# Kernel optimization log

Measured on AMD Instinct MI355X. Metric: run time of the kernel, lower is better.

The kernel has to match this reference:

```python
import jax, jax.numpy as jnp
import numpy as np

K_WIN = 7  # temporal window size (odd)
EPS = 1e-5


def setup_inputs() -> dict:
    key = jax.random.key(0)
    ks = jax.random.split(key, 10)
    B, C, T, H, W = 8, 512, 32, 7, 7
    N, E = 8, 64  # heads, inter channels = C // N
    s = 0.02
    return {
        "x": jax.random.normal(ks[0], (B, C, T, H, W), jnp.float32),
        "gamma": jnp.ones((C,), jnp.float32),
        "beta": jnp.zeros((C,), jnp.float32),
        "Wq": jax.random.normal(ks[1], (N, E, C), jnp.float32) * s,
        "bq": jax.random.normal(ks[2], (N, E), jnp.float32) * s,
        "Wk": jax.random.normal(ks[3], (N, E, C), jnp.float32) * s,
        "bk": jax.random.normal(ks[4], (N, E), jnp.float32) * s,
        "Wv": jax.random.normal(ks[5], (N, E, C), jnp.float32) * s,
        "bv": jax.random.normal(ks[6], (N, E), jnp.float32) * s,
        "Wo": jax.random.normal(ks[7], (N, C, E), jnp.float32) * s,
        "bo": jax.random.normal(ks[8], (N, C), jnp.float32) * s,
    }


def reference(x, gamma, beta, Wq, bq, Wk, bk, Wv, bv, Wo, bo):
    B, C, T, H, W = x.shape
    K = K_WIN
    P = H * W          # spatial positions per frame
    L = K * P          # positions per temporal window

    # BatchNorm3d (training-mode batch stats over B,T,H,W)
    mean = jnp.mean(x, axis=(0, 2, 3, 4), keepdims=True)
    var = jnp.var(x, axis=(0, 2, 3, 4), keepdims=True)
    g = gamma[None, :, None, None, None]
    b = beta[None, :, None, None, None]
    xb = g * (x - mean) * jax.lax.rsqrt(var + EPS) + b  # (B,C,T,H,W)

    # temporal zero-pad so that number of windows S == T
    pad = K // 2
    xp = jnp.pad(xb, ((0, 0), (0, 0), (pad, pad), (0, 0), (0, 0)))
    # gather sliding windows: (B,C,T,K,H,W)
    win_idx = jnp.arange(T)[:, None] + jnp.arange(K)[None, :]
    xw = xp[:, :, win_idx]

    xwf = xw.reshape(B, C, T, L)   # window tokens (key/value source)
    xcf = xb.reshape(B, C, T, P)   # center frame (query source)

    # per-head projections (dropout is identity in eval mode)
    q = jnp.einsum('nec,bctp->bntep', Wq, xcf) + bq[None, :, None, :, None]
    k = jnp.einsum('nec,bctl->bntel', Wk, xwf) + bk[None, :, None, :, None]
    v = jnp.einsum('nec,bctl->bntel', Wv, xwf) + bv[None, :, None, :, None]

    # attention: scores (B,N,T,P,L), softmax over window positions L (no scaling, as in original)
    alpha = jnp.einsum('bntep,bntel->bntpl', q, k)
    alpha = jax.nn.softmax(alpha, axis=-1)
    y = jnp.einsum('bntpl,bntel->bntep', alpha, v)

    # output projection per head, then mean over heads
    out = jnp.einsum('nce,bntep->bntcp', Wo, y) + bo[None, :, None, :, None]
    z = jnp.mean(out, axis=1)                 # (B,T,C,P)
    z = jnp.transpose(z, (0, 2, 1, 3)).reshape(B, C, T, H, W)
    return z + xb  # residual with BN output
```

## Files before the change

kernel.cpp:

```cpp
#include <hip/hip_runtime.h>
#include <hip/hip_bf16.h>


typedef float f32x4 __attribute__((ext_vector_type(4)));
typedef short s16x8 __attribute__((ext_vector_type(8)));
typedef short s16x4 __attribute__((ext_vector_type(4)));
typedef __bf16 bf16x8 __attribute__((ext_vector_type(8)));

static __device__ __forceinline__ float bf2f(unsigned short u){
  union { unsigned int i; float f; } x; x.i = ((unsigned int)u) << 16; return x.f;
}
static __device__ __forceinline__ unsigned short f2bf(float f){
  union { __hip_bfloat16 h; unsigned short u; } x; x.h = __float2bfloat16(f); return x.u;
}
static __device__ __forceinline__ f32x4 mfma16(s16x8 a, s16x8 b, f32x4 c){
  return __builtin_amdgcn_mfma_f32_16x16x32_bf16(
      __builtin_bit_cast(bf16x8, a), __builtin_bit_cast(bf16x8, b), c, 0, 0, 0);
}
static __device__ __forceinline__ void gload16(const unsigned short* g, unsigned short* l){
  __builtin_amdgcn_global_load_lds(
      (const __attribute__((address_space(1))) unsigned int*)g,
      (__attribute__((address_space(3))) unsigned int*)l, 16, 0, 0);
}
#define VMCNT(N) asm volatile("s_waitcnt vmcnt(" #N ")" ::: "memory")

__global__ __launch_bounds__(256) void stats_kernel(const float* __restrict__ x,
    const float* __restrict__ gamma, const float* __restrict__ beta,
    float* __restrict__ scale, float* __restrict__ shift){
  const int c = blockIdx.x, tid = threadIdx.x;
  float s1 = 0.f, s2 = 0.f;
  const float* xc = x + (size_t)c*1568;
  for (int i = tid; i < 3136; i += 256){
    int b = i / 392, j = i - b*392;
    f32x4 v = *(const f32x4*)(xc + (size_t)b*802816 + j*4);
    s1 += v[0]+v[1]+v[2]+v[3];
    s2 += v[0]*v[0]+v[1]*v[1]+v[2]*v[2]+v[3]*v[3];
  }
  #pragma unroll
  for (int off = 32; off > 0; off >>= 1){
    s1 += __shfl_down(s1, off);
    s2 += __shfl_down(s2, off);
  }
  __shared__ float r1[4], r2[4];
  int wave = tid >> 6, lane = tid & 63;
  if (lane == 0){ r1[wave] = s1; r2[wave] = s2; }
  __syncthreads();
  if (tid == 0){
    float t1 = r1[0]+r1[1]+r1[2]+r1[3];
    float t2 = r2[0]+r2[1]+r2[2]+r2[3];
    const float inv = 1.f/12544.f;
    float mean = t1*inv;
    float var  = t2*inv - mean*mean;
    float sc = gamma[c]*rsqrtf(var + 1e-5f);
    scale[c] = sc;
    shift[c] = beta[c] - mean*sc;
  }
}

__global__ __launch_bounds__(512) void pack_kernel(const float* __restrict__ Wq,
    const float* __restrict__ Wk, const float* __restrict__ Wv,
    const float* __restrict__ Wo, const float* __restrict__ bo,
    unsigned short* __restrict__ Wall, unsigned short* __restrict__ Wo2,
    float* __restrict__ bo_sum){
  int i = blockIdx.x*512 + threadIdx.x;
  if (i < 786432){
    const float* W = (i < 262144) ? Wq : (i < 524288 ? Wk : Wv);
    Wall[i] = f2bf(W[i & 262143]);
  } else if (i < 1048576){
    int j = i - 786432;
    int c = j >> 9, k = j & 511, nn = k >> 6, e = k & 63;
    Wo2[j] = f2bf(Wo[((size_t)nn*512 + c)*64 + e] * 0.125f);
  } else if (i < 1049088){
    int c = i - 1048576;
    float s = 0.f;
    #pragma unroll
    for (int nn = 0; nn < 8; ++nn) s += bo[nn*512 + c];
    bo_sum[c] = s * 0.125f;
  }
}

__global__ __launch_bounds__(256) void xt_kernel(const float* __restrict__ x,
    const float* __restrict__ scale, const float* __restrict__ shift,
    unsigned short* __restrict__ Xt){
  __shared__ unsigned short Xc[512][52];
  const int bt = blockIdx.x, b = bt >> 5, t = bt & 31, tid = threadIdx.x;
  const float* xb = x + (size_t)b*802816 + t*49;
  for (int i = tid; i < 512*49; i += 256){
    int c = i / 49, p = i - c*49;
    Xc[c][p] = f2bf(xb[(size_t)c*1568 + p]*scale[c] + shift[c]);
  }
  __syncthreads();
  unsigned short* dst = Xt + (size_t)bt*32768;
  for (int i = tid; i < 4096; i += 256){
    int p = i & 63, c0 = (i >> 6) << 3;
    s16x8 v;
    #pragma unroll
    for (int j = 0; j < 8; ++j) v[j] = (p < 49) ? (short)Xc[c0+j][p] : (short)0;
    *(s16x8*)(dst + p*512 + c0) = v;
  }
}

__global__ __launch_bounds__(256) void qkv_gemm(const unsigned short* __restrict__ Wall,
    const unsigned short* __restrict__ Xt,
    const float* __restrict__ bq, const float* __restrict__ bk, const float* __restrict__ bv,
    unsigned short* __restrict__ Qg, unsigned short* __restrict__ Kg,
    unsigned short* __restrict__ Vg){
  __shared__ unsigned short As[4][4096];
  __shared__ unsigned short Bs[4][4096];
  const int bid = blockIdx.x;
  const int id = (bid & 7)*192 + (bid >> 3);
  const int bm = id % 12, bn = id / 12;
  const int m0 = bm*128, n0 = bn*128;
  const int tid = threadIdx.x;
  const int w = __builtin_amdgcn_readfirstlane(tid >> 6);
  const int lane = tid & 63, l15 = lane & 15, g = lane >> 4, g4 = (lane >> 4)*4;
  const int wm = w >> 1, wn = w & 1;
  const int cA = w*128 + lane;
  int offA[4], offB[4];
  #pragma unroll
  for (int mi = 0; mi < 4; ++mi){
    int row = wm*64 + mi*16 + l15;
    offA[mi] = row*32 + ((g ^ ((row>>1)&3))<<3);
  }
  #pragma unroll
  for (int ni = 0; ni < 4; ++ni){
    int col = wn*64 + ni*16 + l15;
    offB[ni] = col*32 + ((g ^ ((col>>1)&3))<<3);
  }
  f32x4 acc[4][4];
  #pragma unroll
  for (int mi = 0; mi < 4; ++mi)
    #pragma unroll
    for (int ni = 0; ni < 4; ++ni) acc[mi][ni] = 0.f;

  auto stage = [&](int bufi, int ks){
    #pragma unroll
    for (int it = 0; it < 2; ++it){
      int c = cA + it*64;
      int row = c >> 2, slot = c & 3;
      int ko = ks*32 + ((slot ^ ((row>>1)&3))<<3);
      gload16(Wall + (size_t)(m0 + row)*512 + ko, &As[bufi][(w*128 + it*64)*8]);
      gload16(Xt   + (size_t)(n0 + row)*512 + ko, &Bs[bufi][(w*128 + it*64)*8]);
    }
  };
  auto compute = [&](int bufi){
    s16x8 Af[4], Bf[4];
    #pragma unroll
    for (int mi = 0; mi < 4; ++mi) Af[mi] = *(const s16x8*)&As[bufi][offA[mi]];
    #pragma unroll
    for (int ni = 0; ni < 4; ++ni) Bf[ni] = *(const s16x8*)&Bs[bufi][offB[ni]];
    #pragma unroll
    for (int mi = 0; mi < 4; ++mi)
      #pragma unroll
      for (int ni = 0; ni < 4; ++ni)
        acc[mi][ni] = mfma16(Af[mi], Bf[ni], acc[mi][ni]);
  };

  stage(0, 0); stage(1, 1); stage(2, 2);
  #pragma unroll 1
  for (int j = 0; j < 13; ++j){
    VMCNT(8);
    __builtin_amdgcn_s_barrier();
    __builtin_amdgcn_sched_barrier(0);
    stage((j+3) & 3, j+3);
    __builtin_amdgcn_s_setprio(1);
    compute(j & 3);
    __builtin_amdgcn_s_setprio(0);
  }
  VMCNT(8);  __builtin_amdgcn_s_barrier(); __builtin_amdgcn_sched_barrier(0);
  __builtin_amdgcn_s_setprio(1); compute(1); __builtin_amdgcn_s_setprio(0);
  VMCNT(4);  __builtin_amdgcn_s_barrier(); __builtin_amdgcn_sched_barrier(0);
  __builtin_amdgcn_s_setprio(1); compute(2); __builtin_amdgcn_s_setprio(0);
  VMCNT(0);  __builtin_amdgcn_s_barrier(); __builtin_amdgcn_sched_barrier(0);
  __builtin_amdgcn_s_setprio(1); compute(3); __builtin_amdgcn_s_setprio(0);

  const int qb = bm*2 + wm;
  const int which = qb >> 3, n = qb & 7;
  const int bt = bn*2 + wn, b = bt >> 5, t = bt & 31;
  const size_t bnt = ((size_t)(b*8 + n)*32 + t);
  const float* bias = which == 0 ? bq : (which == 1 ? bk : bv);
  #pragma unroll
  for (int mi = 0; mi < 4; ++mi){
    const int e0 = mi*16 + g4;
    const f32x4 bb = *(const f32x4*)(bias + n*64 + e0);
    #pragma unroll
    for (int ni = 0; ni < 4; ++ni){
      const int p = ni*16 + l15;
      f32x4 v = acc[mi][ni] + bb;
      if (which == 0) v *= 1.4426950408889634f;
      if (p < 49){
        if (which < 2){
          s16x4 u;
          #pragma unroll
          for (int r = 0; r < 4; ++r) u[r] = (short)f2bf(v[r]);
          *(s16x4*)((which == 0 ? Qg : Kg) + (bnt*49 + p)*64 + e0) = u;
        } else {
          #pragma unroll
          for (int r = 0; r < 4; ++r)
            Vg[bnt*3328 + (size_t)(e0 + r)*52 + p] = f2bf(v[r]);
        }
      }
    }
  }
}

__global__ __launch_bounds__(512,2) void attn_kernel(const unsigned short* __restrict__ Qg,
    const unsigned short* __restrict__ Kg, const unsigned short* __restrict__ Vg,
    const float* __restrict__ bk, const float* __restrict__ bv,
    unsigned short* __restrict__ Yg){
  const int bid = blockIdx.x;
  const int bt = ((bid & 7) << 5) | (bid >> 3);
  const int b = bt >> 5, t = bt & 31, tid = threadIdx.x;
  const int n = __builtin_amdgcn_readfirstlane(tid >> 6);
  const int lane = tid & 63, g = lane >> 4, l15 = lane & 15, g4 = (lane >> 4)*4;
  const size_t bnt = ((size_t)(b*8 + n)*32 + t);
  const unsigned short* Qb = Qg + bnt*3136;
  s16x8 Qf[4][2];
  #pragma unroll
  for (int ni = 0; ni < 4; ++ni)
    #pragma unroll
    for (int ks = 0; ks < 2; ++ks)
      Qf[ni][ks] = *(const s16x8*)(Qb + (ni*16 + l15)*64 + ks*32 + g*8);
  const float* bkp = bk + n*64;
  f32x4 bkf[2][2];
  bkf[0][0] = *(const f32x4*)(bkp + g*8);      bkf[0][1] = *(const f32x4*)(bkp + g*8 + 4);
  bkf[1][0] = *(const f32x4*)(bkp + 32 + g*8); bkf[1][1] = *(const f32x4*)(bkp + 32 + g*8 + 4);
  float pad_l[4];
  #pragma unroll
  for (int ni = 0; ni < 4; ++ni){
    float s = 0.f;
    #pragma unroll
    for (int ks = 0; ks < 2; ++ks)
      #pragma unroll
      for (int h = 0; h < 2; ++h)
        #pragma unroll
        for (int j = 0; j < 4; ++j)
          s += bf2f((unsigned short)Qf[ni][ks][h*4+j]) * bkf[ks][h][j];
    s += __shfl_xor(s, 16); s += __shfl_xor(s, 32);
    pad_l[ni] = s;
  }
  float m_run[4], d_run[4];
  f32x4 Yacc[4][4];
  #pragma unroll
  for (int ni = 0; ni < 4; ++ni){
    m_run[ni] = -1e30f; d_run[ni] = 0.f;
    #pragma unroll
    for (int me = 0; me < 4; ++me) Yacc[me][ni] = 0.f;
  }
  int slo = 3 - t; if (slo < 0) slo = 0;
  int shi = 34 - t; if (shi > 6) shi = 6;
  for (int s = slo; s <= shi; ++s){
    const int tt = t + s - 3;
    const unsigned short* Kb = Kg + ((size_t)(b*8 + n)*32 + tt)*3136;
    const unsigned short* Vb = Vg + ((size_t)(b*8 + n)*32 + tt)*3328;
    f32x4 S[4][4];
    #pragma unroll
    for (int mi = 0; mi < 4; ++mi)
      #pragma unroll
      for (int ni = 0; ni < 4; ++ni) S[mi][ni] = 0.f;
    __builtin_amdgcn_s_setprio(1);
    #pragma unroll
    for (int ks = 0; ks < 2; ++ks)
      #pragma unroll
      for (int mi = 0; mi < 4; ++mi){
        s16x8 Kf = *(const s16x8*)(Kb + (mi*16 + l15)*64 + ks*32 + g*8);
        #pragma unroll
        for (int ni = 0; ni < 4; ++ni)
          S[mi][ni] = mfma16(Kf, Qf[ni][ks], S[mi][ni]);
      }
    __builtin_amdgcn_s_setprio(0);
    #pragma unroll
    for (int r = 0; r < 4; ++r){
      const bool bad = (g4 + r) >= 1;
      #pragma unroll
      for (int ni = 0; ni < 4; ++ni)
        S[3][ni][r] = bad ? -1e30f : S[3][ni][r];
    }
    #pragma unroll
    for (int ni = 0; ni < 4; ++ni){
      float mx = -1e30f;
      #pragma unroll
      for (int mi = 0; mi < 4; ++mi)
        #pragma unroll
        for (int r = 0; r < 4; ++r) mx = fmaxf(mx, S[mi][ni][r]);
      mx = fmaxf(mx, __shfl_xor(mx, 16));
      mx = fmaxf(mx, __shfl_xor(mx, 32));
      const float mn = fmaxf(m_run[ni], mx);
      const float rs = exp2f(m_run[ni] - mn);
      m_run[ni] = mn;
      float sum = 0.f;
      #pragma unroll
      for (int mi = 0; mi < 4; ++mi)
        #pragma unroll
        for (int r = 0; r < 4; ++r){
          float e = exp2f(S[mi][ni][r] - mn);
          S[mi][ni][r] = e; sum += e;
        }
      sum += __shfl_xor(sum, 16); sum += __shfl_xor(sum, 32);
      d_run[ni] = d_run[ni]*rs + sum;
      #pragma unroll
      for (int me = 0; me < 4; ++me) Yacc[me][ni] *= rs;
    }
    #pragma unroll
    for (int ks = 0; ks < 2; ++ks){
      s16x8 Pf[4];
      #pragma unroll
      for (int ni = 0; ni < 4; ++ni){
        f32x4 a = S[2*ks][ni], b2 = S[2*ks+1][ni];
        s16x8 pf;
        #pragma unroll
        for (int j = 0; j < 4; ++j){
          pf[j]   = (short)f2bf(a[j]);
          pf[4+j] = (short)f2bf(b2[j]);
        }
        Pf[ni] = pf;
      }
      __builtin_amdgcn_s_setprio(1);
      #pragma unroll
      for (int me = 0; me < 4; ++me){
        s16x4 vlo = *(const s16x4*)(Vb + (size_t)(me*16 + l15)*52 + ks*32 + g4);
        s16x4 vhi = *(const s16x4*)(Vb + (size_t)(me*16 + l15)*52 + ks*32 + 16 + g4);
        s16x8 Vf;
        #pragma unroll
        for (int j = 0; j < 4; ++j){ Vf[j] = vlo[j]; Vf[4+j] = vhi[j]; }
        #pragma unroll
        for (int ni = 0; ni < 4; ++ni)
          Yacc[me][ni] = mfma16(Vf, Pf[ni], Yacc[me][ni]);
      }
      __builtin_amdgcn_s_setprio(0);
    }
  }
  const int n_pad = slo + (6 - shi);
  f32x4 bvf[4];
  #pragma unroll
  for (int me = 0; me < 4; ++me)
    bvf[me] = *(const f32x4*)(bv + n*64 + me*16 + g4);
  unsigned short* Yb = Yg + bnt*3136;
  #pragma unroll
  for (int ni = 0; ni < 4; ++ni){
    float rs = 1.f, pw = 0.f, d = d_run[ni];
    if (n_pad > 0){
      const float mf = fmaxf(m_run[ni], pad_l[ni]);
      rs = exp2f(m_run[ni] - mf);
      pw = (float)(n_pad*49) * exp2f(pad_l[ni] - mf);
      d = d_run[ni]*rs + pw;
    }
    const float inv = 1.f/d;
    const int p = ni*16 + l15;
    if (p < 49){
      #pragma unroll
      for (int me = 0; me < 4; ++me){
        s16x4 u;
        #pragma unroll
        for (int r = 0; r < 4; ++r)
          u[r] = (short)f2bf((Yacc[me][ni][r]*rs + pw*bvf[me][r])*inv);
        *(s16x4*)(Yb + (size_t)p*64 + me*16 + g4) = u;
      }
    }
  }
}

__global__ __launch_bounds__(256) void out_gemm(const unsigned short* __restrict__ Wo2,
    const unsigned short* __restrict__ Yg, const unsigned short* __restrict__ Xt,
    const float* __restrict__ scale, const float* __restrict__ shift,
    const float* __restrict__ bo_sum, float* __restrict__ out){
  __shared__ unsigned short As[4][4096];
  __shared__ unsigned short Bs[4][4096];
  const int bid = blockIdx.x;
  const int id = (bid & 7)*64 + (bid >> 3);
  const int bm = id % 4, bn = id / 4;
  const int m0 = bm*128, n0 = bn*128;
  const int tid = threadIdx.x;
  const int w = __builtin_amdgcn_readfirstlane(tid >> 6);
  const int lane = tid & 63, l15 = lane & 15, g = lane >> 4, g4 = (lane >> 4)*4;
  const int wm = w >> 1, wn = w & 1;
  const int cA = w*128 + lane;
  int offA[4], offB[4];
  #pragma unroll
  for (int mi = 0; mi < 4; ++mi){
    int row = wm*64 + mi*16 + l15;
    offA[mi] = row*32 + ((g ^ ((row>>1)&3))<<3);
  }
  #pragma unroll
  for (int ni = 0; ni < 4; ++ni){
    int col = wn*64 + ni*16 + l15;
    offB[ni] = col*32 + ((g ^ ((col>>1)&3))<<3);
  }
  f32x4 acc[4][4];
  #pragma unroll
  for (int mi = 0; mi < 4; ++mi)
    #pragma unroll
    for (int ni = 0; ni < 4; ++ni) acc[mi][ni] = 0.f;

  auto stage = [&](int bufi, int ks){
    const int nh = ks >> 1, eo = (ks & 1)*32;
    #pragma unroll
    for (int it = 0; it < 2; ++it){
      int c = cA + it*64;
      int row = c >> 2, slot = c & 3;
      int sw = ((slot ^ ((row>>1)&3))<<3);
      gload16(Wo2 + (size_t)(m0 + row)*512 + ks*32 + sw, &As[bufi][(w*128 + it*64)*8]);
      const int col = n0 + row, btc = col >> 6, p = col & 63;
      const size_t bb = ((size_t)((btc >> 5)*8 + nh)*32 + (btc & 31));
      gload16(Yg + bb*3136 + p*64 + eo + sw, &Bs[bufi][(w*128 + it*64)*8]);
    }
  };
  auto compute = [&](int bufi){
    s16x8 Af[4], Bf[4];
    #pragma unroll
    for (int mi = 0; mi < 4; ++mi) Af[mi] = *(const s16x8*)&As[bufi][offA[mi]];
    #pragma unroll
    for (int ni = 0; ni < 4; ++ni) Bf[ni] = *(const s16x8*)&Bs[bufi][offB[ni]];
    #pragma unroll
    for (int mi = 0; mi < 4; ++mi)
      #pragma unroll
      for (int ni = 0; ni < 4; ++ni)
        acc[mi][ni] = mfma16(Af[mi], Bf[ni], acc[mi][ni]);
  };

  stage(0, 0); stage(1, 1); stage(2, 2);
  #pragma unroll 1
  for (int j = 0; j < 13; ++j){
    VMCNT(8);
    __builtin_amdgcn_s_barrier();
    __builtin_amdgcn_sched_barrier(0);
    stage((j+3) & 3, j+3);
    __builtin_amdgcn_s_setprio(1);
    compute(j & 3);
    __builtin_amdgcn_s_setprio(0);
  }
  VMCNT(8);  __builtin_amdgcn_s_barrier(); __builtin_amdgcn_sched_barrier(0);
  __builtin_amdgcn_s_setprio(1); compute(1); __builtin_amdgcn_s_setprio(0);
  VMCNT(4);  __builtin_amdgcn_s_barrier(); __builtin_amdgcn_sched_barrier(0);
  __builtin_amdgcn_s_setprio(1); compute(2); __builtin_amdgcn_s_setprio(0);
  VMCNT(0);  __builtin_amdgcn_s_barrier(); __builtin_amdgcn_sched_barrier(0);
  __builtin_amdgcn_s_setprio(1); compute(3); __builtin_amdgcn_s_setprio(0);

  const int cb = m0 + wm*64;
  const int bt = bn*2 + wn, b = bt >> 5, t = bt & 31;
  const unsigned short* XtB = Xt + (size_t)bt*32768;
  #pragma unroll
  for (int mi = 0; mi < 4; ++mi){
    const int c0 = cb + mi*16 + g4;
    const f32x4 sc = *(const f32x4*)(bo_sum + c0);
    #pragma unroll
    for (int ni = 0; ni < 4; ++ni){
      const int p = ni*16 + l15;
      if (p < 49){
        s16x4 xb = *(const s16x4*)(XtB + p*512 + c0);
        #pragma unroll
        for (int r = 0; r < 4; ++r){
          const int c = c0 + r;
          out[((size_t)(b*512 + c))*1568 + t*49 + p] =
              acc[mi][ni][r] + sc[r] + bf2f((unsigned short)xb[r]);
        }
      }
    }
  }
}

extern "C" void kernel_launch(void* const* d_in, const int* in_sizes, int n_in_,
                              void* d_out, int out_size, void* d_ws, size_t ws_size,
                              hipStream_t stream){
  const float* x     = (const float*)d_in[0];
  const float* gamma = (const float*)d_in[1];
  const float* beta  = (const float*)d_in[2];
  const float* Wq    = (const float*)d_in[3];
  const float* bq    = (const float*)d_in[4];
  const float* Wk    = (const float*)d_in[5];
  const float* bk    = (const float*)d_in[6];
  const float* Wv    = (const float*)d_in[7];
  const float* bv    = (const float*)d_in[8];
  const float* Wo    = (const float*)d_in[9];
  const float* bo    = (const float*)d_in[10];
  float* out = (float*)d_out;

  char* ws = (char*)d_ws;
  float* scale  = (float*)ws;
  float* shift  = scale + 512;
  float* bo_sum = shift + 512;
  unsigned short* Wall = (unsigned short*)(ws + 8192);
  const size_t PAD = 16384;
  unsigned short* Wo2 = Wall + 786432;
  unsigned short* Xt  = Wo2 + 262144;
  unsigned short* Qg  = Xt + 8388608;
  unsigned short* Kg  = Qg + 6422528 + PAD;
  unsigned short* Vg  = Kg + 6422528 + PAD;
  unsigned short* Yg  = Vg + 6815744 + PAD;

  hipLaunchKernelGGL(stats_kernel, dim3(512), dim3(256), 0, stream,
                     x, gamma, beta, scale, shift);
  hipLaunchKernelGGL(pack_kernel, dim3(2049), dim3(512), 0, stream,
                     Wq, Wk, Wv, Wo, bo, Wall, Wo2, bo_sum);
  hipLaunchKernelGGL(xt_kernel, dim3(256), dim3(256), 0, stream,
                     x, scale, shift, Xt);
  hipLaunchKernelGGL(qkv_gemm, dim3(1536), dim3(256), 0, stream,
                     Wall, Xt, bq, bk, bv, Qg, Kg, Vg);
  hipLaunchKernelGGL(attn_kernel, dim3(256), dim3(512), 0, stream,
                     Qg, Kg, Vg, bk, bv, Yg);
  hipLaunchKernelGGL(out_gemm, dim3(512), dim3(256), 0, stream,
                     Wo2, Yg, Xt, scale, shift, bo_sum, out);
}
```

Measured before the change: 130.7 us.

## Enlarge QKV GEMM tile to 256x128 and switch both GEMMs to 3-stage pipelines

The QKV GEMM now computes a 256x128 output tile per block, with each wave holding 8x4 MFMA accumulators, so each staged X tile is reused across twice as many weight rows and the grid halves. Both GEMMs move from a 4-buffer to a 3-buffer LDS ring with a two-stage prefetch and request two blocks per CU via launch bounds. Together these cut LDS footprint and global B-operand traffic. In exchange they add register pressure from the larger accumulator, give less latency hiding per block, and leave fewer blocks to balance across CUs.

```diff
diff --git a/kernel.cpp b/kernel.cpp
--- a/kernel.cpp
+++ b/kernel.cpp
@@ -100,26 +100,25 @@
   }
 }
 
-__global__ __launch_bounds__(256) void qkv_gemm(const unsigned short* __restrict__ Wall,
+__global__ __launch_bounds__(256,2) void qkv_gemm(const unsigned short* __restrict__ Wall,
     const unsigned short* __restrict__ Xt,
     const float* __restrict__ bq, const float* __restrict__ bk, const float* __restrict__ bv,
     unsigned short* __restrict__ Qg, unsigned short* __restrict__ Kg,
     unsigned short* __restrict__ Vg){
-  __shared__ unsigned short As[4][4096];
-  __shared__ unsigned short Bs[4][4096];
+  __shared__ unsigned short As[3][8192];
+  __shared__ unsigned short Bs[3][4096];
   const int bid = blockIdx.x;
-  const int id = (bid & 7)*192 + (bid >> 3);
-  const int bm = id % 12, bn = id / 12;
-  const int m0 = bm*128, n0 = bn*128;
+  const int id = (bid & 7)*96 + (bid >> 3);
+  const int bm = id % 6, bn = id / 6;
+  const int m0 = bm*256, n0 = bn*128;
   const int tid = threadIdx.x;
   const int w = __builtin_amdgcn_readfirstlane(tid >> 6);
   const int lane = tid & 63, l15 = lane & 15, g = lane >> 4, g4 = (lane >> 4)*4;
   const int wm = w >> 1, wn = w & 1;
-  const int cA = w*128 + lane;
-  int offA[4], offB[4];
-  #pragma unroll
-  for (int mi = 0; mi < 4; ++mi){
-    int row = wm*64 + mi*16 + l15;
+  int offA[8], offB[4];
+  #pragma unroll
+  for (int mi = 0; mi < 8; ++mi){
+    int row = wm*128 + mi*16 + l15;
     offA[mi] = row*32 + ((g ^ ((row>>1)&3))<<3);
   }
   #pragma unroll
@@ -127,61 +126,65 @@
     int col = wn*64 + ni*16 + l15;
     offB[ni] = col*32 + ((g ^ ((col>>1)&3))<<3);
   }
-  f32x4 acc[4][4];
-  #pragma unroll
-  for (int mi = 0; mi < 4; ++mi)
+  f32x4 acc[8][4];
+  #pragma unroll
+  for (int mi = 0; mi < 8; ++mi)
     #pragma unroll
     for (int ni = 0; ni < 4; ++ni) acc[mi][ni] = 0.f;
 
-  auto stage = [&](int bufi, int ks){
+  auto stage = [&](int bufi, int kk){
+    #pragma unroll
+    for (int it = 0; it < 4; ++it){
+      int slot = it*256 + tid;
+      int row = slot >> 2, q = slot & 3;
+      int ko = kk*32 + ((q ^ ((row>>1)&3))<<3);
+      gload16(Wall + (size_t)(m0 + row)*512 + ko, &As[bufi][(it*256 + w*64)*8]);
+    }
     #pragma unroll
     for (int it = 0; it < 2; ++it){
-      int c = cA + it*64;
-      int row = c >> 2, slot = c & 3;
-      int ko = ks*32 + ((slot ^ ((row>>1)&3))<<3);
-      gload16(Wall + (size_t)(m0 + row)*512 + ko, &As[bufi][(w*128 + it*64)*8]);
-      gload16(Xt   + (size_t)(n0 + row)*512 + ko, &Bs[bufi][(w*128 + it*64)*8]);
+      int slot = it*256 + tid;
+      int row = slot >> 2, q = slot & 3;
+      int ko = kk*32 + ((q ^ ((row>>1)&3))<<3);
+      gload16(Xt + (size_t)(n0 + row)*512 + ko, &Bs[bufi][(it*256 + w*64)*8]);
     }
   };
   auto compute = [&](int bufi){
-    s16x8 Af[4], Bf[4];
-    #pragma unroll
-    for (int mi = 0; mi < 4; ++mi) Af[mi] = *(const s16x8*)&As[bufi][offA[mi]];
+    s16x8 Af[8], Bf[4];
+    #pragma unroll
+    for (int mi = 0; mi < 8; ++mi) Af[mi] = *(const s16x8*)&As[bufi][offA[mi]];
     #pragma unroll
     for (int ni = 0; ni < 4; ++ni) Bf[ni] = *(const s16x8*)&Bs[bufi][offB[ni]];
     #pragma unroll
-    for (int mi = 0; mi < 4; ++mi)
+    for (int mi = 0; mi < 8; ++mi)
       #pragma unroll
       for (int ni = 0; ni < 4; ++ni)
         acc[mi][ni] = mfma16(Af[mi], Bf[ni], acc[mi][ni]);
   };
 
-  stage(0, 0); stage(1, 1); stage(2, 2);
+  stage(0, 0); stage(1, 1);
   #pragma unroll 1
-  for (int j = 0; j < 13; ++j){
-    VMCNT(8);
+  for (int j = 0; j < 14; ++j){
+    VMCNT(6);
     __builtin_amdgcn_s_barrier();
+    stage((j+2)%3, j+2);
     __builtin_amdgcn_sched_barrier(0);
-    stage((j+3) & 3, j+3);
     __builtin_amdgcn_s_setprio(1);
-    compute(j & 3);
+    compute(j%3);
     __builtin_amdgcn_s_setprio(0);
   }
-  VMCNT(8);  __builtin_amdgcn_s_barrier(); __builtin_amdgcn_sched_barrier(0);
-  __builtin_amdgcn_s_setprio(1); compute(1); __builtin_amdgcn_s_setprio(0);
-  VMCNT(4);  __builtin_amdgcn_s_barrier(); __builtin_amdgcn_sched_barrier(0);
+  VMCNT(6); __builtin_amdgcn_s_barrier();
   __builtin_amdgcn_s_setprio(1); compute(2); __builtin_amdgcn_s_setprio(0);
-  VMCNT(0);  __builtin_amdgcn_s_barrier(); __builtin_amdgcn_sched_barrier(0);
-  __builtin_amdgcn_s_setprio(1); compute(3); __builtin_amdgcn_s_setprio(0);
-
-  const int qb = bm*2 + wm;
-  const int which = qb >> 3, n = qb & 7;
+  VMCNT(0); __builtin_amdgcn_s_barrier();
+  __builtin_amdgcn_s_setprio(1); compute(0); __builtin_amdgcn_s_setprio(0);
+
   const int bt = bn*2 + wn, b = bt >> 5, t = bt & 31;
-  const size_t bnt = ((size_t)(b*8 + n)*32 + t);
-  const float* bias = which == 0 ? bq : (which == 1 ? bk : bv);
-  #pragma unroll
-  for (int mi = 0; mi < 4; ++mi){
-    const int e0 = mi*16 + g4;
+  #pragma unroll
+  for (int mi = 0; mi < 8; ++mi){
+    const int qb = bm*4 + wm*2 + (mi >> 2);
+    const int which = qb >> 3, n = qb & 7;
+    const int e0 = (mi & 3)*16 + g4;
+    const size_t bnt = ((size_t)(b*8 + n)*32 + t);
+    const float* bias = which == 0 ? bq : (which == 1 ? bk : bv);
     const f32x4 bb = *(const f32x4*)(bias + n*64 + e0);
     #pragma unroll
     for (int ni = 0; ni < 4; ++ni){
@@ -360,12 +363,12 @@
   }
 }
 
-__global__ __launch_bounds__(256) void out_gemm(const unsigned short* __restrict__ Wo2,
+__global__ __launch_bounds__(256,2) void out_gemm(const unsigned short* __restrict__ Wo2,
     const unsigned short* __restrict__ Yg, const unsigned short* __restrict__ Xt,
     const float* __restrict__ scale, const float* __restrict__ shift,
     const float* __restrict__ bo_sum, float* __restrict__ out){
-  __shared__ unsigned short As[4][4096];
-  __shared__ unsigned short Bs[4][4096];
+  __shared__ unsigned short As[3][4096];
+  __shared__ unsigned short Bs[3][4096];
   const int bid = blockIdx.x;
   const int id = (bid & 7)*64 + (bid >> 3);
   const int bm = id % 4, bn = id / 4;
@@ -418,23 +421,21 @@
         acc[mi][ni] = mfma16(Af[mi], Bf[ni], acc[mi][ni]);
   };
 
-  stage(0, 0); stage(1, 1); stage(2, 2);
+  stage(0, 0); stage(1, 1);
   #pragma unroll 1
-  for (int j = 0; j < 13; ++j){
-    VMCNT(8);
+  for (int j = 0; j < 14; ++j){
+    VMCNT(4);
     __builtin_amdgcn_s_barrier();
+    stage((j+2)%3, j+2);
     __builtin_amdgcn_sched_barrier(0);
-    stage((j+3) & 3, j+3);
     __builtin_amdgcn_s_setprio(1);
-    compute(j & 3);
+    compute(j%3);
     __builtin_amdgcn_s_setprio(0);
   }
-  VMCNT(8);  __builtin_amdgcn_s_barrier(); __builtin_amdgcn_sched_barrier(0);
-  __builtin_amdgcn_s_setprio(1); compute(1); __builtin_amdgcn_s_setprio(0);
-  VMCNT(4);  __builtin_amdgcn_s_barrier(); __builtin_amdgcn_sched_barrier(0);
+  VMCNT(4); __builtin_amdgcn_s_barrier();
   __builtin_amdgcn_s_setprio(1); compute(2); __builtin_amdgcn_s_setprio(0);
-  VMCNT(0);  __builtin_amdgcn_s_barrier(); __builtin_amdgcn_sched_barrier(0);
-  __builtin_amdgcn_s_setprio(1); compute(3); __builtin_amdgcn_s_setprio(0);
+  VMCNT(0); __builtin_amdgcn_s_barrier();
+  __builtin_amdgcn_s_setprio(1); compute(0); __builtin_amdgcn_s_setprio(0);
 
   const int cb = m0 + wm*64;
   const int bt = bn*2 + wn, b = bt >> 5, t = bt & 31;
@@ -494,7 +495,7 @@
                      Wq, Wk, Wv, Wo, bo, Wall, Wo2, bo_sum);
   hipLaunchKernelGGL(xt_kernel, dim3(256), dim3(256), 0, stream,
                      x, scale, shift, Xt);
-  hipLaunchKernelGGL(qkv_gemm, dim3(1536), dim3(256), 0, stream,
+  hipLaunchKernelGGL(qkv_gemm, dim3(768), dim3(256), 0, stream,
                      Wall, Xt, bq, bk, bv, Qg, Kg, Vg);
   hipLaunchKernelGGL(attn_kernel, dim3(256), dim3(512), 0, stream,
                      Qg, Kg, Vg, bk, bv, Yg);
```

Result: no change. 132.4 us (+1.3%).
